# Performance work log

Hardware: AMD Instinct MI355X
Metric: run time of the kernel (lower is better)

Reference implementation:

```python
import jax, jax.numpy as jnp
import numpy as np

N_ITER = 100
EPS = 1e-12


def _corr(x, k):
    # x: [C,H,W], k: [kh,kw]; per-channel 'same' cross-correlation, zero padding
    C = x.shape[0]
    kern = jnp.broadcast_to(k, (C, 1) + k.shape)
    return jax.lax.conv_general_dilated(
        x[None], kern, window_strides=(1, 1), padding='SAME',
        feature_group_count=C,
        dimension_numbers=('NCHW', 'OIHW', 'NCHW'))[0]


def _corr_t(x, k):
    # adjoint of zero-padded 'same' correlation = correlation with flipped kernel
    return _corr(x, k[::-1, ::-1])


def _A(x, kernel, reg_kernels, w2):
    # A x = K^T K x + sum_i w_i^2 R_i^T R_i x
    out = _corr_t(_corr(x, kernel), kernel)
    for i in range(reg_kernels.shape[0]):  # small fixed number of reg kernels
        rk = reg_kernels[i]
        out = out + w2[i] * _corr_t(_corr(x, rk), rk)
    return out


def setup_inputs() -> dict:
    key = jax.random.key(0)
    k1, k2, k3, k4 = jax.random.split(key, 4)
    image = jax.random.uniform(k1, (3, 768, 768), dtype=jnp.float32)
    kernel = jax.random.uniform(k2, (15, 15), dtype=jnp.float32)
    kernel = kernel / jnp.sum(kernel)  # normalized blur PSF
    reg_kernels = jax.random.normal(k3, (2, 5, 5), dtype=jnp.float32)
    reg_kernel_weights = jax.random.uniform(
        k4, (2,), dtype=jnp.float32, minval=1e-6, maxval=1.0)
    return {'image': image, 'kernel': kernel, 'reg_kernels': reg_kernels,
            'reg_kernel_weights': reg_kernel_weights}


def reference(image, kernel, reg_kernels, reg_kernel_weights):
    w2 = reg_kernel_weights ** 2
    # CG init: x0 = image, b = image, solve A x = K^T b
    KTb = _corr_t(image, kernel)
    r0 = KTb - _A(image, kernel, reg_kernels, w2)
    xrp0 = jnp.stack([image, r0, r0])  # [3, C, H, W]: x, r, p

    def body(xrp, _):
        x, r, p = xrp[0], xrp[1], xrp[2]
        Ap = _A(p, kernel, reg_kernels, w2)
        rtr = jnp.sum(r * r, axis=(1, 2), keepdims=True)      # per-channel [C,1,1]
        ptAp = jnp.sum(p * Ap, axis=(1, 2), keepdims=True)
        alpha = rtr / (ptAp + EPS)
        x_new = x + alpha * p
        r_new = r - alpha * Ap
        beta = jnp.sum(r_new * r_new, axis=(1, 2), keepdims=True) / (rtr + EPS)
        p_new = r_new + beta * p
        return jnp.stack([x_new, r_new, p_new]), None

    xrp, _ = jax.lax.scan(jax.checkpoint(body), xrp0, None, length=N_ITER)
    return xrp
```

## Files before the change

kernel.cpp:

```cpp
#include <hip/hip_runtime.h>

#define EPS 1e-12f

constexpr int H = 768, W = 768, C = 3;
constexpr int HW = H * W;
constexpr int CHW = C * HW;

constexpr int TSX = 64, TSY = 32;
constexpr int PTX = TSX + 14;
constexpr int PTY = TSY + 14;
constexpr int LDS1 = 84;
constexpr int PRX = TSX + 4;
constexpr int PRY = TSY + 4;
constexpr int LDS2 = 76;

constexpr int NSLOT = 16;
constexpr int SSTR = 16;
constexpr int SCALSZ = NSLOT * SSTR;

__device__ __forceinline__ float block_reduce_256(float v, float* redbuf) {
    #pragma unroll
    for (int off = 32; off > 0; off >>= 1) v += __shfl_down(v, off, 64);
    const int tid = threadIdx.x;
    if ((tid & 63) == 0) redbuf[tid >> 6] = v;
    __syncthreads();
    return redbuf[0] + redbuf[1] + redbuf[2] + redbuf[3];
}

__device__ __forceinline__ float sum_slots(const float* base, int c) {
    float s = 0.f;
    #pragma unroll
    for (int k = 0; k < NSLOT; ++k) s += base[k * SSTR + c];
    return s;
}

template <int MODE>
__global__ __launch_bounds__(256) void stage1_k(
    const float* __restrict__ in, const float* __restrict__ rvec,
    const float* __restrict__ k15, const float* __restrict__ rks,
    float* __restrict__ t0, float* __restrict__ t1, float* __restrict__ t2,
    float* __restrict__ pout,
    const float* __restrict__ bnum, const float* __restrict__ bden)
{
    __shared__ float sp[PTY * LDS1];
    __shared__ __align__(16) float kt[15 * 16];
    __shared__ __align__(16) float rkt[2 * 5 * 8];
    const int c = blockIdx.z;
    const int bx = blockIdx.x * TSX, by = blockIdx.y * TSY;
    const int tid = threadIdx.x;
    const float* inC = in + c * HW;

    float beta = 0.f;
    if (MODE == 2) {
        const float n = sum_slots(bnum, c), d = sum_slots(bden, c);
        beta = n / (d + EPS);
    }

    if (tid < 240) { const int i = tid >> 4, j = tid & 15; kt[tid] = (j < 15) ? k15[i * 15 + j] : 0.f; }
    if (tid < 80) {
        const int kk = tid / 40, rem = tid % 40, i = rem >> 3, j = rem & 7;
        rkt[tid] = (j < 5) ? rks[kk * 25 + i * 5 + j] : 0.f;
    }

    for (int t = tid; t < PTY * PTX; t += 256) {
        const int ly = t / PTX, lx = t - ly * PTX;
        const int gy = by - 7 + ly, gx = bx - 7 + lx;
        float v = 0.f;
        if ((unsigned)gy < (unsigned)H && (unsigned)gx < (unsigned)W) {
            const int g = gy * W + gx;
            v = inC[g];
            if (MODE == 2) v = rvec[c * HW + g] + beta * v;
        }
        sp[ly * LDS1 + lx] = v;
    }
    __syncthreads();

    const int oy = tid >> 3;
    const int ox = (tid & 7) << 3;

    float acc[8];
    #pragma unroll
    for (int k = 0; k < 8; ++k) acc[k] = 0.f;
    #pragma unroll 1
    for (int i = 0; i < 15; ++i) {
        const float* rowp = sp + (oy + i) * LDS1 + ox;
        float seg[24];
        #pragma unroll
        for (int q = 0; q < 6; ++q) *(float4*)(seg + 4 * q) = *(const float4*)(rowp + 4 * q);
        float kv[16];
        #pragma unroll
        for (int q = 0; q < 4; ++q) *(float4*)(kv + 4 * q) = *(const float4*)(kt + i * 16 + 4 * q);
        #pragma unroll
        for (int j = 0; j < 15; ++j)
            #pragma unroll
            for (int k = 0; k < 8; ++k) acc[k] = fmaf(seg[j + k], kv[j], acc[k]);
    }

    float accB[8], accC[8];
    #pragma unroll
    for (int k = 0; k < 8; ++k) { accB[k] = 0.f; accC[k] = 0.f; }
    #pragma unroll 1
    for (int i = 0; i < 5; ++i) {
        const float* rowp = sp + (oy + 5 + i) * LDS1 + ox + 4;
        float seg[16];
        #pragma unroll
        for (int q = 0; q < 4; ++q) *(float4*)(seg + 4 * q) = *(const float4*)(rowp + 4 * q);
        float kb[8], kc[8];
        *(float4*)(kb) = *(const float4*)(rkt + i * 8);
        *(float4*)(kb + 4) = *(const float4*)(rkt + i * 8 + 4);
        *(float4*)(kc) = *(const float4*)(rkt + 40 + i * 8);
        *(float4*)(kc + 4) = *(const float4*)(rkt + 40 + i * 8 + 4);
        #pragma unroll
        for (int j = 0; j < 5; ++j)
            #pragma unroll
            for (int k = 0; k < 8; ++k) {
                accB[k] = fmaf(seg[1 + k + j], kb[j], accB[k]);
                accC[k] = fmaf(seg[1 + k + j], kc[j], accC[k]);
            }
    }

    const int g = c * HW + (by + oy) * W + bx + ox;
    const float* ctr = sp + (oy + 7) * LDS1 + ox + 7;
    if (MODE == 0) {
        #pragma unroll
        for (int k = 0; k < 8; ++k) acc[k] = ctr[k] - acc[k];
    }
    *(float4*)(t0 + g)     = make_float4(acc[0], acc[1], acc[2], acc[3]);
    *(float4*)(t0 + g + 4) = make_float4(acc[4], acc[5], acc[6], acc[7]);
    *(float4*)(t1 + g)     = make_float4(accB[0], accB[1], accB[2], accB[3]);
    *(float4*)(t1 + g + 4) = make_float4(accB[4], accB[5], accB[6], accB[7]);
    *(float4*)(t2 + g)     = make_float4(accC[0], accC[1], accC[2], accC[3]);
    *(float4*)(t2 + g + 4) = make_float4(accC[4], accC[5], accC[6], accC[7]);
    if (MODE == 2) {
        *(float4*)(pout + g)     = make_float4(ctr[0], ctr[1], ctr[2], ctr[3]);
        *(float4*)(pout + g + 4) = make_float4(ctr[4], ctr[5], ctr[6], ctr[7]);
    }
}

template <int MODE>
__global__ __launch_bounds__(256) void stage2_k(
    const float* __restrict__ t0, const float* __restrict__ t1, const float* __restrict__ t2,
    const float* __restrict__ k15, const float* __restrict__ rks,
    const float* __restrict__ rw,
    const float* __restrict__ img, const float* __restrict__ p,
    float* __restrict__ Ap, float* __restrict__ outR, float* __restrict__ outP0,
    float* __restrict__ outX, float* __restrict__ red)
{
    __shared__ float s0[PTY * LDS1];
    __shared__ float s1[PRY * LDS2];
    __shared__ float s2[PRY * LDS2];
    __shared__ __align__(16) float kt[15 * 16];
    __shared__ __align__(16) float rkt[2 * 5 * 8];
    __shared__ float redbuf[4];
    const int c = blockIdx.z;
    const int bx = blockIdx.x * TSX, by = blockIdx.y * TSY;
    const int tid = threadIdx.x;
    const float* t0C = t0 + c * HW;
    const float* t1C = t1 + c * HW;
    const float* t2C = t2 + c * HW;

    if (tid < 240) { const int i = tid >> 4, j = tid & 15; kt[tid] = (j < 15) ? k15[(14 - i) * 15 + (14 - j)] : 0.f; }
    if (tid < 80) {
        const int kk = tid / 40, rem = tid % 40, i = rem >> 3, j = rem & 7;
        rkt[tid] = (j < 5) ? rks[kk * 25 + (4 - i) * 5 + (4 - j)] : 0.f;
    }

    for (int t = tid; t < PTY * PTX; t += 256) {
        const int ly = t / PTX, lx = t - ly * PTX;
        const int gy = by - 7 + ly, gx = bx - 7 + lx;
        s0[ly * LDS1 + lx] =
            ((unsigned)gy < (unsigned)H && (unsigned)gx < (unsigned)W) ? t0C[gy * W + gx] : 0.f;
    }
    for (int t = tid; t < PRY * PRX; t += 256) {
        const int ly = t / PRX, lx = t - ly * PRX;
        const int gy = by - 2 + ly, gx = bx - 2 + lx;
        float v1 = 0.f, v2 = 0.f;
        if ((unsigned)gy < (unsigned)H && (unsigned)gx < (unsigned)W) {
            const int g = gy * W + gx;
            v1 = t1C[g]; v2 = t2C[g];
        }
        s1[ly * LDS2 + lx] = v1;
        s2[ly * LDS2 + lx] = v2;
    }
    __syncthreads();

    const int oy = tid >> 3;
    const int ox = (tid & 7) << 3;

    float acc[8];
    #pragma unroll
    for (int k = 0; k < 8; ++k) acc[k] = 0.f;
    #pragma unroll 1
    for (int i = 0; i < 15; ++i) {
        const float* rowp = s0 + (oy + i) * LDS1 + ox;
        float seg[24];
        #pragma unroll
        for (int q = 0; q < 6; ++q) *(float4*)(seg + 4 * q) = *(const float4*)(rowp + 4 * q);
        float kv[16];
        #pragma unroll
        for (int q = 0; q < 4; ++q) *(float4*)(kv + 4 * q) = *(const float4*)(kt + i * 16 + 4 * q);
        #pragma unroll
        for (int j = 0; j < 15; ++j)
            #pragma unroll
            for (int k = 0; k < 8; ++k) acc[k] = fmaf(seg[j + k], kv[j], acc[k]);
    }

    float accB[8], accC[8];
    #pragma unroll
    for (int k = 0; k < 8; ++k) { accB[k] = 0.f; accC[k] = 0.f; }
    #pragma unroll 1
    for (int i = 0; i < 5; ++i) {
        const float* r1p = s1 + (oy + i) * LDS2 + ox;
        const float* r2p = s2 + (oy + i) * LDS2 + ox;
        float sA[12], sB[12];
        #pragma unroll
        for (int q = 0; q < 3; ++q) *(float4*)(sA + 4 * q) = *(const float4*)(r1p + 4 * q);
        #pragma unroll
        for (int q = 0; q < 3; ++q) *(float4*)(sB + 4 * q) = *(const float4*)(r2p + 4 * q);
        float kb[8], kc[8];
        *(float4*)(kb) = *(const float4*)(rkt + i * 8);
        *(float4*)(kb + 4) = *(const float4*)(rkt + i * 8 + 4);
        *(float4*)(kc) = *(const float4*)(rkt + 40 + i * 8);
        *(float4*)(kc + 4) = *(const float4*)(rkt + 40 + i * 8 + 4);
        #pragma unroll
        for (int j = 0; j < 5; ++j)
            #pragma unroll
            for (int k = 0; k < 8; ++k) {
                accB[k] = fmaf(sA[k + j], kb[j], accB[k]);
                accC[k] = fmaf(sB[k + j], kc[j], accC[k]);
            }
    }

    const float w0 = rw[0], w1 = rw[1];
    const float sgn = (MODE == 0) ? -1.f : 1.f;
    const float w02 = w0 * w0 * sgn, w12 = w1 * w1 * sgn;
    float v[8];
    #pragma unroll
    for (int k = 0; k < 8; ++k) v[k] = acc[k] + w02 * accB[k] + w12 * accC[k];

    const int g = c * HW + (by + oy) * W + bx + ox;
    float local = 0.f;
    if (MODE == 0) {
        *(float4*)(outR + g)      = make_float4(v[0], v[1], v[2], v[3]);
        *(float4*)(outR + g + 4)  = make_float4(v[4], v[5], v[6], v[7]);
        *(float4*)(outP0 + g)     = make_float4(v[0], v[1], v[2], v[3]);
        *(float4*)(outP0 + g + 4) = make_float4(v[4], v[5], v[6], v[7]);
        *(float4*)(outX + g)      = *(const float4*)(img + g);
        *(float4*)(outX + g + 4)  = *(const float4*)(img + g + 4);
        #pragma unroll
        for (int k = 0; k < 8; ++k) local += v[k] * v[k];
    } else {
        *(float4*)(Ap + g)     = make_float4(v[0], v[1], v[2], v[3]);
        *(float4*)(Ap + g + 4) = make_float4(v[4], v[5], v[6], v[7]);
        const float4 p0 = *(const float4*)(p + g);
        const float4 p1 = *(const float4*)(p + g + 4);
        local = p0.x * v[0] + p0.y * v[1] + p0.z * v[2] + p0.w * v[3]
              + p1.x * v[4] + p1.y * v[5] + p1.z * v[6] + p1.w * v[7];
    }
    const float tot = block_reduce_256(local, redbuf);
    if (tid == 0) {
        const int bid = blockIdx.y * gridDim.x + blockIdx.x;
        atomicAdd(red + (bid & (NSLOT - 1)) * SSTR + c, tot);
    }
}

__global__ __launch_bounds__(256) void cg_update_k(
    float* __restrict__ x, float* __restrict__ r,
    const float* __restrict__ Ap, const float* __restrict__ p,
    const float* __restrict__ rtr_cur, const float* __restrict__ ptap,
    float* __restrict__ rtr_next)
{
    __shared__ float redbuf[4];
    const int c = blockIdx.z;
    const float n = sum_slots(rtr_cur, c), d = sum_slots(ptap, c);
    const float alpha = n / (d + EPS);
    const int idx = c * HW + (blockIdx.x * 256 + threadIdx.x) * 8;
    float local = 0.f;
    #pragma unroll
    for (int h = 0; h < 2; ++h) {
        const int o = idx + 4 * h;
        float4 xv = *(float4*)(x + o);
        float4 rv = *(float4*)(r + o);
        const float4 pv = *(const float4*)(p + o);
        const float4 av = *(const float4*)(Ap + o);
        xv.x = fmaf(alpha, pv.x, xv.x); rv.x = fmaf(-alpha, av.x, rv.x);
        xv.y = fmaf(alpha, pv.y, xv.y); rv.y = fmaf(-alpha, av.y, rv.y);
        xv.z = fmaf(alpha, pv.z, xv.z); rv.z = fmaf(-alpha, av.z, rv.z);
        xv.w = fmaf(alpha, pv.w, xv.w); rv.w = fmaf(-alpha, av.w, rv.w);
        *(float4*)(x + o) = xv;
        *(float4*)(r + o) = rv;
        local += rv.x * rv.x + rv.y * rv.y + rv.z * rv.z + rv.w * rv.w;
    }
    const float tot = block_reduce_256(local, redbuf);
    if (threadIdx.x == 0)
        atomicAdd(rtr_next + ((int)blockIdx.x & (NSLOT - 1)) * SSTR + c, tot);
}

__global__ __launch_bounds__(256) void p_final_k(
    const float* __restrict__ r, const float* __restrict__ p99, float* __restrict__ pout,
    const float* __restrict__ num, const float* __restrict__ den)
{
    const int c = blockIdx.z;
    const float beta = sum_slots(num, c) / (sum_slots(den, c) + EPS);
    const int idx = c * HW + (blockIdx.x * 256 + threadIdx.x) * 8;
    #pragma unroll
    for (int h = 0; h < 2; ++h) {
        const int o = idx + 4 * h;
        const float4 rv = *(const float4*)(r + o);
        const float4 pv = *(const float4*)(p99 + o);
        *(float4*)(pout + o) = make_float4(
            fmaf(beta, pv.x, rv.x), fmaf(beta, pv.y, rv.y),
            fmaf(beta, pv.z, rv.z), fmaf(beta, pv.w, rv.w));
    }
}

extern "C" void kernel_launch(void* const* d_in, const int* in_sizes, int n_in,
                              void* d_out, int out_size, void* d_ws, size_t ws_size,
                              hipStream_t stream)
{
    const float* img = (const float*)d_in[0];
    const float* k15 = (const float*)d_in[1];
    const float* rks = (const float*)d_in[2];
    const float* rw  = (const float*)d_in[3];

    float* out = (float*)d_out;
    float* xs = out;
    float* rs = out + CHW;
    float* ps = out + 2 * CHW;

    float* ws   = (float*)d_ws;
    float* buf0 = ws;
    float* t0   = buf0 + CHW;
    float* t1   = t0 + CHW;
    float* t2   = t1 + CHW;
    float* Ap   = t2 + CHW;
    float* scal = Ap + CHW;
    float* rtr2 = scal;
    float* ptap = scal + 101 * SCALSZ;

    hipMemsetAsync(scal, 0, (size_t)(101 + 100) * SCALSZ * sizeof(float), stream);

    const dim3 gc(W / TSX, H / TSY, C), bc(256);
    const dim3 ge(HW / 2048, 1, C);

    stage1_k<0><<<gc, bc, 0, stream>>>(img, nullptr, k15, rks, t0, t1, t2,
                                       nullptr, nullptr, nullptr);
    stage2_k<0><<<gc, bc, 0, stream>>>(t0, t1, t2, k15, rks, rw, img, nullptr,
                                       nullptr, rs, buf0, xs, rtr2);

    for (int i = 0; i < 100; ++i) {
        float* pin  = (i & 1) ? buf0 : ps;
        float* pcur = (i & 1) ? ps : buf0;
        if (i == 0) {
            stage1_k<1><<<gc, bc, 0, stream>>>(buf0, nullptr, k15, rks, t0, t1, t2,
                                               nullptr, nullptr, nullptr);
        } else {
            stage1_k<2><<<gc, bc, 0, stream>>>(pin, rs, k15, rks, t0, t1, t2,
                                               pcur, rtr2 + i * SCALSZ, rtr2 + (i - 1) * SCALSZ);
        }
        stage2_k<1><<<gc, bc, 0, stream>>>(t0, t1, t2, k15, rks, rw, nullptr, pcur,
                                           Ap, nullptr, nullptr, nullptr, ptap + i * SCALSZ);
        cg_update_k<<<ge, bc, 0, stream>>>(xs, rs, Ap, pcur,
                                           rtr2 + i * SCALSZ, ptap + i * SCALSZ,
                                           rtr2 + (i + 1) * SCALSZ);
    }
    p_final_k<<<ge, bc, 0, stream>>>(rs, ps, ps, rtr2 + 100 * SCALSZ, rtr2 + 99 * SCALSZ);
}
```

Baseline: 8.086 ms.

## Fuse forward and adjoint convolution stages into one kernel with halo recompute

Merges the forward correlation stage and the adjoint correlation stage into a single kernel. Intermediate results stay in shared memory, computed over an enlarged halo region, instead of round-tripping through global buffers t0/t1/t2. This removes the intermediate global traffic and one launch per CG iteration. In exchange it adds redundant convolution work on the halo and a much larger LDS footprint, which may reduce occupancy.

```diff
diff --git a/kernel.cpp b/kernel.cpp
--- a/kernel.cpp
+++ b/kernel.cpp
@@ -6,17 +6,13 @@
 constexpr int HW = H * W;
 constexpr int CHW = C * HW;
 
-constexpr int TSX = 64, TSY = 32;
-constexpr int PTX = TSX + 14;
-constexpr int PTY = TSY + 14;
-constexpr int LDS1 = 84;
-constexpr int PRX = TSX + 4;
-constexpr int PRY = TSY + 4;
-constexpr int LDS2 = 76;
-
 constexpr int NSLOT = 16;
 constexpr int SSTR = 16;
 constexpr int SCALSZ = NSLOT * SSTR;
+
+constexpr int SPW = 100, SPH = 60;
+constexpr int S0W = 84,  S0H = 46;
+constexpr int S1W = 76,  S1H = 36;
 
 __device__ __forceinline__ float block_reduce_256(float v, float* redbuf) {
     #pragma unroll
@@ -35,43 +31,129 @@
 }
 
 template <int MODE>
-__global__ __launch_bounds__(256) void stage1_k(
+__global__ __launch_bounds__(256) void fusedA_k(
     const float* __restrict__ in, const float* __restrict__ rvec,
     const float* __restrict__ k15, const float* __restrict__ rks,
-    float* __restrict__ t0, float* __restrict__ t1, float* __restrict__ t2,
-    float* __restrict__ pout,
-    const float* __restrict__ bnum, const float* __restrict__ bden)
+    const float* __restrict__ rw,
+    float* __restrict__ Ap, float* __restrict__ outR,
+    float* __restrict__ outP, float* __restrict__ outX,
+    const float* __restrict__ bnum, const float* __restrict__ bden,
+    float* __restrict__ red)
 {
-    __shared__ float sp[PTY * LDS1];
-    __shared__ __align__(16) float kt[15 * 16];
-    __shared__ __align__(16) float rkt[2 * 5 * 8];
+    __shared__ __align__(16) float sp[SPH * SPW];
+    __shared__ __align__(16) float st0[S0H * S0W];
+    __shared__ __align__(16) float st1[S1H * S1W];
+    __shared__ __align__(16) float st2[S1H * S1W];
+    __shared__ __align__(16) float kt[240], ktf[240];
+    __shared__ __align__(16) float rkt[80], rktf[80];
+    __shared__ float redbuf[4];
+
     const int c = blockIdx.z;
-    const int bx = blockIdx.x * TSX, by = blockIdx.y * TSY;
+    const int bx = blockIdx.x * 64, by = blockIdx.y * 32;
     const int tid = threadIdx.x;
     const float* inC = in + c * HW;
 
     float beta = 0.f;
-    if (MODE == 2) {
-        const float n = sum_slots(bnum, c), d = sum_slots(bden, c);
-        beta = n / (d + EPS);
-    }
-
-    if (tid < 240) { const int i = tid >> 4, j = tid & 15; kt[tid] = (j < 15) ? k15[i * 15 + j] : 0.f; }
+    if (MODE == 2) beta = sum_slots(bnum, c) / (sum_slots(bden, c) + EPS);
+
+    if (tid < 240) {
+        const int i = tid >> 4, j = tid & 15;
+        kt[tid]  = (j < 15) ? k15[i * 15 + j] : 0.f;
+        ktf[tid] = (j < 15) ? k15[(14 - i) * 15 + (14 - j)] : 0.f;
+    }
     if (tid < 80) {
         const int kk = tid / 40, rem = tid % 40, i = rem >> 3, j = rem & 7;
-        rkt[tid] = (j < 5) ? rks[kk * 25 + i * 5 + j] : 0.f;
-    }
-
-    for (int t = tid; t < PTY * PTX; t += 256) {
-        const int ly = t / PTX, lx = t - ly * PTX;
-        const int gy = by - 7 + ly, gx = bx - 7 + lx;
+        rkt[tid]  = (j < 5) ? rks[kk * 25 + i * 5 + j] : 0.f;
+        rktf[tid] = (j < 5) ? rks[kk * 25 + (4 - i) * 5 + (4 - j)] : 0.f;
+    }
+
+    for (int t = tid; t < SPH * 96; t += 256) {
+        const int ly = t / 96, lx = t - ly * 96;
+        const int gy = by - 14 + ly, gx = bx - 14 + lx;
         float v = 0.f;
         if ((unsigned)gy < (unsigned)H && (unsigned)gx < (unsigned)W) {
             const int g = gy * W + gx;
             v = inC[g];
             if (MODE == 2) v = rvec[c * HW + g] + beta * v;
         }
-        sp[ly * LDS1 + lx] = v;
+        sp[ly * SPW + lx] = v;
+    }
+    __syncthreads();
+
+    for (int s = tid; s < 460; s += 256) {
+        const int row = s / 10;
+        const int col8 = (s - row * 10) << 3;
+        float acc[8];
+        #pragma unroll
+        for (int k = 0; k < 8; ++k) acc[k] = 0.f;
+        #pragma unroll 1
+        for (int i = 0; i < 15; ++i) {
+            const float* rowp = sp + (row + i) * SPW + col8;
+            float seg[24];
+            #pragma unroll
+            for (int q = 0; q < 6; ++q) *(float4*)(seg + 4 * q) = *(const float4*)(rowp + 4 * q);
+            float kv[16];
+            #pragma unroll
+            for (int q = 0; q < 4; ++q) *(float4*)(kv + 4 * q) = *(const float4*)(kt + i * 16 + 4 * q);
+            #pragma unroll
+            for (int j = 0; j < 15; ++j)
+                #pragma unroll
+                for (int k = 0; k < 8; ++k) acc[k] = fmaf(seg[j + k], kv[j], acc[k]);
+        }
+        const int gy = by - 7 + row, gxb = bx - 7 + col8;
+        if ((unsigned)gy >= (unsigned)H) {
+            #pragma unroll
+            for (int k = 0; k < 8; ++k) acc[k] = 0.f;
+        } else {
+            #pragma unroll
+            for (int k = 0; k < 8; ++k)
+                if ((unsigned)(gxb + k) >= (unsigned)W) acc[k] = 0.f;
+        }
+        float* o = st0 + row * S0W + col8;
+        *(float4*)(o)     = make_float4(acc[0], acc[1], acc[2], acc[3]);
+        *(float4*)(o + 4) = make_float4(acc[4], acc[5], acc[6], acc[7]);
+    }
+
+    for (int s = tid; s < 324; s += 256) {
+        const int row = s / 9;
+        const int col8 = (s - row * 9) << 3;
+        float accB[8], accC[8];
+        #pragma unroll
+        for (int k = 0; k < 8; ++k) { accB[k] = 0.f; accC[k] = 0.f; }
+        #pragma unroll 1
+        for (int i = 0; i < 5; ++i) {
+            const float* rowp = sp + (row + 10 + i) * SPW + col8 + 8;
+            float seg[16];
+            #pragma unroll
+            for (int q = 0; q < 4; ++q) *(float4*)(seg + 4 * q) = *(const float4*)(rowp + 4 * q);
+            float kb[8], kc[8];
+            *(float4*)(kb)     = *(const float4*)(rkt + i * 8);
+            *(float4*)(kb + 4) = *(const float4*)(rkt + i * 8 + 4);
+            *(float4*)(kc)     = *(const float4*)(rkt + 40 + i * 8);
+            *(float4*)(kc + 4) = *(const float4*)(rkt + 40 + i * 8 + 4);
+            #pragma unroll
+            for (int j = 0; j < 5; ++j)
+                #pragma unroll
+                for (int k = 0; k < 8; ++k) {
+                    accB[k] = fmaf(seg[j + k + 2], kb[j], accB[k]);
+                    accC[k] = fmaf(seg[j + k + 2], kc[j], accC[k]);
+                }
+        }
+        const int gy = by - 2 + row, gxb = bx - 2 + col8;
+        if ((unsigned)gy >= (unsigned)H) {
+            #pragma unroll
+            for (int k = 0; k < 8; ++k) { accB[k] = 0.f; accC[k] = 0.f; }
+        } else {
+            #pragma unroll
+            for (int k = 0; k < 8; ++k)
+                if ((unsigned)(gxb + k) >= (unsigned)W) { accB[k] = 0.f; accC[k] = 0.f; }
+        }
+        float* o1 = st1 + row * S1W + col8;
+        float* o2 = st2 + row * S1W + col8;
+        *(float4*)(o1)     = make_float4(accB[0], accB[1], accB[2], accB[3]);
+        *(float4*)(o1 + 4) = make_float4(accB[4], accB[5], accB[6], accB[7]);
+        *(float4*)(o2)     = make_float4(accC[0], accC[1], accC[2], accC[3]);
+        *(float4*)(o2 + 4) = make_float4(accC[4], accC[5], accC[6], accC[7]);
     }
     __syncthreads();
 
@@ -83,13 +165,13 @@
     for (int k = 0; k < 8; ++k) acc[k] = 0.f;
     #pragma unroll 1
     for (int i = 0; i < 15; ++i) {
-        const float* rowp = sp + (oy + i) * LDS1 + ox;
+        const float* rowp = st0 + (oy + i) * S0W + ox;
         float seg[24];
         #pragma unroll
         for (int q = 0; q < 6; ++q) *(float4*)(seg + 4 * q) = *(const float4*)(rowp + 4 * q);
         float kv[16];
         #pragma unroll
-        for (int q = 0; q < 4; ++q) *(float4*)(kv + 4 * q) = *(const float4*)(kt + i * 16 + 4 * q);
+        for (int q = 0; q < 4; ++q) *(float4*)(kv + 4 * q) = *(const float4*)(ktf + i * 16 + 4 * q);
         #pragma unroll
         for (int j = 0; j < 15; ++j)
             #pragma unroll
@@ -101,161 +183,76 @@
     for (int k = 0; k < 8; ++k) { accB[k] = 0.f; accC[k] = 0.f; }
     #pragma unroll 1
     for (int i = 0; i < 5; ++i) {
-        const float* rowp = sp + (oy + 5 + i) * LDS1 + ox + 4;
-        float seg[16];
-        #pragma unroll
-        for (int q = 0; q < 4; ++q) *(float4*)(seg + 4 * q) = *(const float4*)(rowp + 4 * q);
-        float kb[8], kc[8];
-        *(float4*)(kb) = *(const float4*)(rkt + i * 8);
-        *(float4*)(kb + 4) = *(const float4*)(rkt + i * 8 + 4);
-        *(float4*)(kc) = *(const float4*)(rkt + 40 + i * 8);
-        *(float4*)(kc + 4) = *(const float4*)(rkt + 40 + i * 8 + 4);
-        #pragma unroll
-        for (int j = 0; j < 5; ++j)
-            #pragma unroll
-            for (int k = 0; k < 8; ++k) {
-                accB[k] = fmaf(seg[1 + k + j], kb[j], accB[k]);
-                accC[k] = fmaf(seg[1 + k + j], kc[j], accC[k]);
-            }
-    }
-
-    const int g = c * HW + (by + oy) * W + bx + ox;
-    const float* ctr = sp + (oy + 7) * LDS1 + ox + 7;
-    if (MODE == 0) {
-        #pragma unroll
-        for (int k = 0; k < 8; ++k) acc[k] = ctr[k] - acc[k];
-    }
-    *(float4*)(t0 + g)     = make_float4(acc[0], acc[1], acc[2], acc[3]);
-    *(float4*)(t0 + g + 4) = make_float4(acc[4], acc[5], acc[6], acc[7]);
-    *(float4*)(t1 + g)     = make_float4(accB[0], accB[1], accB[2], accB[3]);
-    *(float4*)(t1 + g + 4) = make_float4(accB[4], accB[5], accB[6], accB[7]);
-    *(float4*)(t2 + g)     = make_float4(accC[0], accC[1], accC[2], accC[3]);
-    *(float4*)(t2 + g + 4) = make_float4(accC[4], accC[5], accC[6], accC[7]);
-    if (MODE == 2) {
-        *(float4*)(pout + g)     = make_float4(ctr[0], ctr[1], ctr[2], ctr[3]);
-        *(float4*)(pout + g + 4) = make_float4(ctr[4], ctr[5], ctr[6], ctr[7]);
-    }
-}
-
-template <int MODE>
-__global__ __launch_bounds__(256) void stage2_k(
-    const float* __restrict__ t0, const float* __restrict__ t1, const float* __restrict__ t2,
-    const float* __restrict__ k15, const float* __restrict__ rks,
-    const float* __restrict__ rw,
-    const float* __restrict__ img, const float* __restrict__ p,
-    float* __restrict__ Ap, float* __restrict__ outR, float* __restrict__ outP0,
-    float* __restrict__ outX, float* __restrict__ red)
-{
-    __shared__ float s0[PTY * LDS1];
-    __shared__ float s1[PRY * LDS2];
-    __shared__ float s2[PRY * LDS2];
-    __shared__ __align__(16) float kt[15 * 16];
-    __shared__ __align__(16) float rkt[2 * 5 * 8];
-    __shared__ float redbuf[4];
-    const int c = blockIdx.z;
-    const int bx = blockIdx.x * TSX, by = blockIdx.y * TSY;
-    const int tid = threadIdx.x;
-    const float* t0C = t0 + c * HW;
-    const float* t1C = t1 + c * HW;
-    const float* t2C = t2 + c * HW;
-
-    if (tid < 240) { const int i = tid >> 4, j = tid & 15; kt[tid] = (j < 15) ? k15[(14 - i) * 15 + (14 - j)] : 0.f; }
-    if (tid < 80) {
-        const int kk = tid / 40, rem = tid % 40, i = rem >> 3, j = rem & 7;
-        rkt[tid] = (j < 5) ? rks[kk * 25 + (4 - i) * 5 + (4 - j)] : 0.f;
-    }
-
-    for (int t = tid; t < PTY * PTX; t += 256) {
-        const int ly = t / PTX, lx = t - ly * PTX;
-        const int gy = by - 7 + ly, gx = bx - 7 + lx;
-        s0[ly * LDS1 + lx] =
-            ((unsigned)gy < (unsigned)H && (unsigned)gx < (unsigned)W) ? t0C[gy * W + gx] : 0.f;
-    }
-    for (int t = tid; t < PRY * PRX; t += 256) {
-        const int ly = t / PRX, lx = t - ly * PRX;
-        const int gy = by - 2 + ly, gx = bx - 2 + lx;
-        float v1 = 0.f, v2 = 0.f;
-        if ((unsigned)gy < (unsigned)H && (unsigned)gx < (unsigned)W) {
-            const int g = gy * W + gx;
-            v1 = t1C[g]; v2 = t2C[g];
-        }
-        s1[ly * LDS2 + lx] = v1;
-        s2[ly * LDS2 + lx] = v2;
-    }
-    __syncthreads();
-
-    const int oy = tid >> 3;
-    const int ox = (tid & 7) << 3;
-
-    float acc[8];
-    #pragma unroll
-    for (int k = 0; k < 8; ++k) acc[k] = 0.f;
-    #pragma unroll 1
-    for (int i = 0; i < 15; ++i) {
-        const float* rowp = s0 + (oy + i) * LDS1 + ox;
-        float seg[24];
-        #pragma unroll
-        for (int q = 0; q < 6; ++q) *(float4*)(seg + 4 * q) = *(const float4*)(rowp + 4 * q);
-        float kv[16];
-        #pragma unroll
-        for (int q = 0; q < 4; ++q) *(float4*)(kv + 4 * q) = *(const float4*)(kt + i * 16 + 4 * q);
-        #pragma unroll
-        for (int j = 0; j < 15; ++j)
-            #pragma unroll
-            for (int k = 0; k < 8; ++k) acc[k] = fmaf(seg[j + k], kv[j], acc[k]);
-    }
-
-    float accB[8], accC[8];
-    #pragma unroll
-    for (int k = 0; k < 8; ++k) { accB[k] = 0.f; accC[k] = 0.f; }
-    #pragma unroll 1
-    for (int i = 0; i < 5; ++i) {
-        const float* r1p = s1 + (oy + i) * LDS2 + ox;
-        const float* r2p = s2 + (oy + i) * LDS2 + ox;
+        const float* r1p = st1 + (oy + i) * S1W + ox;
+        const float* r2p = st2 + (oy + i) * S1W + ox;
         float sA[12], sB[12];
         #pragma unroll
         for (int q = 0; q < 3; ++q) *(float4*)(sA + 4 * q) = *(const float4*)(r1p + 4 * q);
         #pragma unroll
         for (int q = 0; q < 3; ++q) *(float4*)(sB + 4 * q) = *(const float4*)(r2p + 4 * q);
         float kb[8], kc[8];
-        *(float4*)(kb) = *(const float4*)(rkt + i * 8);
-        *(float4*)(kb + 4) = *(const float4*)(rkt + i * 8 + 4);
-        *(float4*)(kc) = *(const float4*)(rkt + 40 + i * 8);
-        *(float4*)(kc + 4) = *(const float4*)(rkt + 40 + i * 8 + 4);
+        *(float4*)(kb)     = *(const float4*)(rktf + i * 8);
+        *(float4*)(kb + 4) = *(const float4*)(rktf + i * 8 + 4);
+        *(float4*)(kc)     = *(const float4*)(rktf + 40 + i * 8);
+        *(float4*)(kc + 4) = *(const float4*)(rktf + 40 + i * 8 + 4);
         #pragma unroll
         for (int j = 0; j < 5; ++j)
             #pragma unroll
             for (int k = 0; k < 8; ++k) {
-                accB[k] = fmaf(sA[k + j], kb[j], accB[k]);
-                accC[k] = fmaf(sB[k + j], kc[j], accC[k]);
+                accB[k] = fmaf(sA[j + k], kb[j], accB[k]);
+                accC[k] = fmaf(sB[j + k], kc[j], accC[k]);
             }
     }
 
+    float vimg[8];
+    if (MODE == 0) {
+        #pragma unroll
+        for (int k = 0; k < 8; ++k) vimg[k] = 0.f;
+        #pragma unroll 1
+        for (int i = 0; i < 15; ++i) {
+            const float* rowp = sp + (oy + 7 + i) * SPW + ox + 4;
+            float seg[28];
+            #pragma unroll
+            for (int q = 0; q < 7; ++q) *(float4*)(seg + 4 * q) = *(const float4*)(rowp + 4 * q);
+            float kv[16];
+            #pragma unroll
+            for (int q = 0; q < 4; ++q) *(float4*)(kv + 4 * q) = *(const float4*)(ktf + i * 16 + 4 * q);
+            #pragma unroll
+            for (int j = 0; j < 15; ++j)
+                #pragma unroll
+                for (int k = 0; k < 8; ++k) vimg[k] = fmaf(seg[j + k + 3], kv[j], vimg[k]);
+        }
+    }
+
     const float w0 = rw[0], w1 = rw[1];
-    const float sgn = (MODE == 0) ? -1.f : 1.f;
-    const float w02 = w0 * w0 * sgn, w12 = w1 * w1 * sgn;
+    const float w02 = w0 * w0, w12 = w1 * w1;
     float v[8];
     #pragma unroll
     for (int k = 0; k < 8; ++k) v[k] = acc[k] + w02 * accB[k] + w12 * accC[k];
 
     const int g = c * HW + (by + oy) * W + bx + ox;
+    const float* ctr = sp + (oy + 14) * SPW + ox + 14;
     float local = 0.f;
     if (MODE == 0) {
-        *(float4*)(outR + g)      = make_float4(v[0], v[1], v[2], v[3]);
-        *(float4*)(outR + g + 4)  = make_float4(v[4], v[5], v[6], v[7]);
-        *(float4*)(outP0 + g)     = make_float4(v[0], v[1], v[2], v[3]);
-        *(float4*)(outP0 + g + 4) = make_float4(v[4], v[5], v[6], v[7]);
-        *(float4*)(outX + g)      = *(const float4*)(img + g);
-        *(float4*)(outX + g + 4)  = *(const float4*)(img + g + 4);
+        #pragma unroll
+        for (int k = 0; k < 8; ++k) v[k] = vimg[k] - v[k];
+        *(float4*)(outR + g)     = make_float4(v[0], v[1], v[2], v[3]);
+        *(float4*)(outR + g + 4) = make_float4(v[4], v[5], v[6], v[7]);
+        *(float4*)(outP + g)     = make_float4(v[0], v[1], v[2], v[3]);
+        *(float4*)(outP + g + 4) = make_float4(v[4], v[5], v[6], v[7]);
+        *(float4*)(outX + g)     = make_float4(ctr[0], ctr[1], ctr[2], ctr[3]);
+        *(float4*)(outX + g + 4) = make_float4(ctr[4], ctr[5], ctr[6], ctr[7]);
         #pragma unroll
         for (int k = 0; k < 8; ++k) local += v[k] * v[k];
     } else {
         *(float4*)(Ap + g)     = make_float4(v[0], v[1], v[2], v[3]);
         *(float4*)(Ap + g + 4) = make_float4(v[4], v[5], v[6], v[7]);
-        const float4 p0 = *(const float4*)(p + g);
-        const float4 p1 = *(const float4*)(p + g + 4);
-        local = p0.x * v[0] + p0.y * v[1] + p0.z * v[2] + p0.w * v[3]
-              + p1.x * v[4] + p1.y * v[5] + p1.z * v[6] + p1.w * v[7];
+        #pragma unroll
+        for (int k = 0; k < 8; ++k) local += ctr[k] * v[k];
+        if (MODE == 2) {
+            *(float4*)(outP + g)     = make_float4(ctr[0], ctr[1], ctr[2], ctr[3]);
+            *(float4*)(outP + g + 4) = make_float4(ctr[4], ctr[5], ctr[6], ctr[7]);
+        }
     }
     const float tot = block_reduce_256(local, redbuf);
     if (tid == 0) {
@@ -330,36 +327,33 @@
 
     float* ws   = (float*)d_ws;
     float* buf0 = ws;
-    float* t0   = buf0 + CHW;
-    float* t1   = t0 + CHW;
-    float* t2   = t1 + CHW;
-    float* Ap   = t2 + CHW;
+    float* Ap   = buf0 + CHW;
     float* scal = Ap + CHW;
     float* rtr2 = scal;
     float* ptap = scal + 101 * SCALSZ;
 
     hipMemsetAsync(scal, 0, (size_t)(101 + 100) * SCALSZ * sizeof(float), stream);
 
-    const dim3 gc(W / TSX, H / TSY, C), bc(256);
+    const dim3 gc(W / 64, H / 32, C), bc(256);
     const dim3 ge(HW / 2048, 1, C);
 
-    stage1_k<0><<<gc, bc, 0, stream>>>(img, nullptr, k15, rks, t0, t1, t2,
-                                       nullptr, nullptr, nullptr);
-    stage2_k<0><<<gc, bc, 0, stream>>>(t0, t1, t2, k15, rks, rw, img, nullptr,
-                                       nullptr, rs, buf0, xs, rtr2);
+    fusedA_k<0><<<gc, bc, 0, stream>>>(img, nullptr, k15, rks, rw,
+                                       nullptr, rs, buf0, xs,
+                                       nullptr, nullptr, rtr2);
 
     for (int i = 0; i < 100; ++i) {
         float* pin  = (i & 1) ? buf0 : ps;
         float* pcur = (i & 1) ? ps : buf0;
         if (i == 0) {
-            stage1_k<1><<<gc, bc, 0, stream>>>(buf0, nullptr, k15, rks, t0, t1, t2,
-                                               nullptr, nullptr, nullptr);
+            fusedA_k<1><<<gc, bc, 0, stream>>>(buf0, nullptr, k15, rks, rw,
+                                               Ap, nullptr, nullptr, nullptr,
+                                               nullptr, nullptr, ptap);
         } else {
-            stage1_k<2><<<gc, bc, 0, stream>>>(pin, rs, k15, rks, t0, t1, t2,
-                                               pcur, rtr2 + i * SCALSZ, rtr2 + (i - 1) * SCALSZ);
-        }
-        stage2_k<1><<<gc, bc, 0, stream>>>(t0, t1, t2, k15, rks, rw, nullptr, pcur,
-                                           Ap, nullptr, nullptr, nullptr, ptap + i * SCALSZ);
+            fusedA_k<2><<<gc, bc, 0, stream>>>(pin, rs, k15, rks, rw,
+                                               Ap, nullptr, pcur, nullptr,
+                                               rtr2 + i * SCALSZ, rtr2 + (i - 1) * SCALSZ,
+                                               ptap + i * SCALSZ);
+        }
         cg_update_k<<<ge, bc, 0, stream>>>(xs, rs, Ap, pcur,
                                            rtr2 + i * SCALSZ, ptap + i * SCALSZ,
                                            rtr2 + (i + 1) * SCALSZ);
```

After: 10.70 ms. +32.3%, slower.
